# Kernel optimization log

Measured on AMD Instinct MI355X. Metric: run time of the kernel, lower is better.

The kernel has to match this reference:

```python
import jax, jax.numpy as jnp
import numpy as np

T, N, E = 4, 20000, 640000
D_IN, D_OUT = 256, 128
RRELU_SLOPE = (1.0 / 8.0 + 1.0 / 3.0) / 2.0  # RReLU eval-mode slope


def setup_inputs() -> dict:
    key = jax.random.key(0)
    ks = jax.random.split(key, 16)

    def glorot(k, shape):
        lim = np.sqrt(6.0 / (shape[0] + shape[1]))
        return jax.random.uniform(k, shape, jnp.float32, -lim, lim)

    node_embs = jax.random.normal(ks[0], (T, N, D_IN), jnp.float32)
    edge_index = jax.random.randint(ks[1], (T, 2, E), 0, N, jnp.int32)
    edge_weight = jax.random.uniform(ks[2], (T, E), jnp.float32)
    mask = jnp.zeros((T, N), jnp.float32)
    return {
        "node_embs": node_embs,
        "edge_index": edge_index,
        "edge_weight": edge_weight,
        "mask": mask,
        "p": glorot(ks[3], (D_IN, 1)),
        "Wz": glorot(ks[4], (D_IN, D_IN)),
        "Uz": glorot(ks[5], (D_IN, D_IN)),
        "bz": jnp.zeros((D_IN, D_OUT), jnp.float32),
        "Wr": glorot(ks[6], (D_IN, D_IN)),
        "Ur": glorot(ks[7], (D_IN, D_IN)),
        "br": jnp.zeros((D_IN, D_OUT), jnp.float32),
        "Wh": glorot(ks[8], (D_IN, D_IN)),
        "Uh": glorot(ks[9], (D_IN, D_IN)),
        "bh": jnp.zeros((D_IN, D_OUT), jnp.float32),
        "W0": glorot(ks[10], (D_IN, D_OUT)),
    }


def reference(node_embs, edge_index, edge_weight, mask, p, Wz, Uz, bz, Wr, Ur, br, Wh, Uh, bh, W0):
    n = node_embs.shape[1]
    k = W0.shape[1]

    def step(W, inputs):
        x, ei, w, m = inputs  # x: [N, D_IN]
        # --- TopK summary (EvolveGCN-H) ---
        scores = (x @ p)[:, 0] / jnp.linalg.norm(p) + m  # [N]
        vals, idx = jax.lax.top_k(scores, k)
        xt = (x[idx] * jnp.tanh(vals)[:, None]).T  # [D_IN, k]
        # --- matrix GRU cell: hidden state is the GCN weight W ---
        z = jax.nn.sigmoid(Wz @ xt + Uz @ W + bz)
        r = jax.nn.sigmoid(Wr @ xt + Ur @ W + br)
        h = jnp.tanh(Wh @ xt + Uh @ (r * W) + bh)
        Wn = (1.0 - z) * W + z * h  # [D_IN, D_OUT]
        # --- sparse GCN conv: adj @ (x @ Wn) ---
        y = x @ Wn  # [N, D_OUT]
        dst, src = ei[0], ei[1]
        agg = jax.ops.segment_sum(w[:, None] * y[src], dst, num_segments=n)
        out = jnp.where(agg >= 0, agg, RRELU_SLOPE * agg)
        return Wn, out

    _, out_seq = jax.lax.scan(step, W0, (node_embs, edge_index, edge_weight, mask))
    return out_seq  # [T, N, D_OUT]
```

## Files before the change

kernel.cpp:

```cpp
#include <hip/hip_runtime.h>

typedef unsigned short u16;
typedef unsigned int u32;
typedef unsigned long long u64;

#define T_ 4
#define N_ 20000
#define E_ 640000
#define DIN 256
#define DOUT 128
#define NT (T_*N_)
#define TE (T_*E_)
#define SLOPE 0.22916666666666666f

#define NB 125
#define BNODES 160
#define CAP 5632
#define NBTOT (T_*NB)

#define SGRAN 11
#define NSB 10
#define NBIN (BNODES*NSB)
#define NBIN_PAD 2048

typedef __attribute__((ext_vector_type(8))) short short8;
typedef __attribute__((ext_vector_type(4))) float f32x4;

__device__ __forceinline__ float blo(u32 u) { return __uint_as_float(u << 16); }
__device__ __forceinline__ float bhi(u32 u) { return __uint_as_float(u & 0xFFFF0000u); }
__device__ __forceinline__ u16 f2bf(float f) {
    u32 u = __float_as_uint(f);
    return (u16)((u + 0x7FFFu + ((u >> 16) & 1u)) >> 16);
}
__device__ __forceinline__ u32 fkey(float f) {
    u32 u = __float_as_uint(f);
    return (u & 0x80000000u) ? ~u : (u | 0x80000000u);
}
__device__ __forceinline__ float fkeyinv(u32 k) {
    u32 u = (k & 0x80000000u) ? (k ^ 0x80000000u) : ~k;
    return __uint_as_float(u);
}

__global__ void k_transpose(const float* Wz, const float* Uz, const float* Wr, const float* Ur,
                            const float* Wh, const float* Uh, u32* Tp) {
    int bid = blockIdx.x;
    int m = bid >> 7, b = bid & 127;
    int idx = b * 256 + threadIdx.x;
    int d2 = idx & 127, i = idx >> 7;
    const float* src;
    switch (m) {
        case 0: src = Wz; break;
        case 1: src = Uz; break;
        case 2: src = Wr; break;
        case 3: src = Ur; break;
        case 4: src = Wh; break;
        default: src = Uh; break;
    }
    float lo = src[i * 256 + 2 * d2];
    float hi = src[i * 256 + 2 * d2 + 1];
    Tp[m * 32768 + d2 * 256 + i] = (u32)f2bf(lo) | ((u32)f2bf(hi) << 16);
}

__global__ __launch_bounds__(256) void k_scores(const float* x, const float* p, const float* mask,
                                                float* scores, u16* xb16) {
    __shared__ float pl[256];
    __shared__ float s_invn;
    int tid = threadIdx.x;
    pl[tid] = p[tid];
    __syncthreads();
    if (tid < 64) {
        float v = pl[tid] * pl[tid] + pl[tid + 64] * pl[tid + 64] +
                  pl[tid + 128] * pl[tid + 128] + pl[tid + 192] * pl[tid + 192];
        for (int o = 32; o > 0; o >>= 1) v += __shfl_xor(v, o);
        if (tid == 0) s_invn = 1.0f / sqrtf(v);
    }
    __syncthreads();
    int wid = tid >> 6, lane = tid & 63;
    for (int it = 0; it < 4; ++it) {
        int node = blockIdx.x * 16 + wid * 4 + it;
        const float* row = x + (size_t)node * DIN + lane * 4;
        float4 u = *(const float4*)row;
        float d = u.x * pl[lane * 4 + 0] + u.y * pl[lane * 4 + 1] +
                  u.z * pl[lane * 4 + 2] + u.w * pl[lane * 4 + 3];
        u32 p0 = (u32)f2bf(u.x) | ((u32)f2bf(u.y) << 16);
        u32 p1 = (u32)f2bf(u.z) | ((u32)f2bf(u.w) << 16);
        *(uint2*)(xb16 + (size_t)node * DIN + lane * 4) = make_uint2(p0, p1);
        for (int o = 32; o > 0; o >>= 1) d += __shfl_xor(d, o);
        if (lane == 0) scores[node] = d * s_invn + mask[node];
    }
}

__global__ __launch_bounds__(256) void k_bin(const int* ei, const float* ew,
                                             int* gcur, uint2* binned) {
    int blk = blockIdx.x;
    int t = blk / 250, ci = blk - t * 250;
    int ebase = ci * 2560;
    int tid = threadIdx.x;
    __shared__ u32 hist[128], sc[128], gbase[128];
    __shared__ uint2 stage[2560];
    if (tid < 128) hist[tid] = 0;
    __syncthreads();
    u32 px[10]; u32 pw[10]; u16 rk[10];
#pragma unroll
    for (int k = 0; k < 10; ++k) {
        int e = ebase + tid + k * 256;
        int dst = ei[t * (2 * E_) + e];
        int src = ei[t * (2 * E_) + E_ + e];
        float w = ew[t * E_ + e];
        int b = dst / BNODES;
        int dl = dst - b * BNODES;
        px[k] = (u32)(t * N_ + src) | ((u32)dl << 17) | ((u32)b << 25);
        pw[k] = __float_as_uint(w);
        rk[k] = (u16)atomicAdd(&hist[b], 1u);
    }
    __syncthreads();
    if (tid < 128) sc[tid] = hist[tid];
    __syncthreads();
    for (int o = 1; o < 128; o <<= 1) {
        u32 v = 0;
        if (tid < 128) { v = sc[tid]; if (tid >= o) v += sc[tid - o]; }
        __syncthreads();
        if (tid < 128) sc[tid] = v;
        __syncthreads();
    }
    if (tid < NB) gbase[tid] = (u32)atomicAdd(&gcur[t * NB + tid], (int)hist[tid]);
#pragma unroll
    for (int k = 0; k < 10; ++k) {
        int b = px[k] >> 25;
        u32 slot = (sc[b] - hist[b]) + rk[k];
        stage[slot] = make_uint2(px[k], pw[k]);
    }
    __syncthreads();
    for (int s = tid; s < 2560; s += 256) {
        uint2 v = stage[s];
        int b = v.x >> 25;
        u32 local = gbase[b] + ((u32)s - (sc[b] - hist[b]));
        if (local < CAP)
            binned[(size_t)(t * NB + b) * CAP + local] = v;
    }
}

__global__ __launch_bounds__(512) void k_scatter(const int* gcur, uint2* binned, int* offsets) {
    int bg = blockIdx.x;
    int t = bg / NB, bl = bg - t * NB;
    uint2* bucket = binned + (size_t)bg * CAP;
    int cnt = gcur[bg]; if (cnt > CAP) cnt = CAP;
    int tid = threadIdx.x;
    int tbase = t * N_;
    __shared__ u32 nhist[NBIN_PAD];
    __shared__ u32 binstart[NBIN_PAD];
    __shared__ u32 wsum[8];
    for (int i = tid; i < NBIN_PAD; i += 512) nhist[i] = 0;
    __syncthreads();
    u32 vx[11]; u32 vw[11]; u16 r_[11]; u16 bn_[11];
#pragma unroll
    for (int k = 0; k < 11; ++k) {
        int e = tid + k * 512;
        r_[k] = 0xFFFFu;
        if (e < cnt) {
            uint2 v = bucket[e];
            vx[k] = v.x; vw[k] = v.y;
            int dl = (v.x >> 17) & 255;
            int s = (int)(v.x & 0x1FFFFu) - tbase;
            int bin = dl * NSB + (s >> SGRAN);
            bn_[k] = (u16)bin;
            r_[k] = (u16)atomicAdd(&nhist[bin], 1u);
        }
    }
    __syncthreads();
    u32 loc1, loc2, loc3, tsum;
    {
        int b0 = tid * 4;
        u32 a = nhist[b0], b = nhist[b0 + 1], c = nhist[b0 + 2], d = nhist[b0 + 3];
        loc1 = a; loc2 = a + b; loc3 = a + b + c; tsum = a + b + c + d;
    }
    int lane = tid & 63, wv = tid >> 6;
    u32 xsc = tsum;
    for (int o = 1; o < 64; o <<= 1) { u32 yv = __shfl_up(xsc, o); if (lane >= o) xsc += yv; }
    if (lane == 63) wsum[wv] = xsc;
    __syncthreads();
    u32 wpre = 0;
    for (int wq = 0; wq < wv; ++wq) wpre += wsum[wq];
    u32 tpre = wpre + xsc - tsum;
    {
        int b0 = tid * 4;
        binstart[b0] = tpre;
        binstart[b0 + 1] = tpre + loc1;
        binstart[b0 + 2] = tpre + loc2;
        binstart[b0 + 3] = tpre + loc3;
    }
    __syncthreads();
    if (tid < BNODES)
        offsets[t * N_ + bl * BNODES + tid] = bg * CAP + (int)binstart[tid * NSB];
    if (bg == NBTOT - 1 && tid == 0) offsets[NT] = NBTOT * CAP;
#pragma unroll
    for (int k = 0; k < 11; ++k) {
        if (r_[k] != 0xFFFFu) {
            u32 pos = binstart[bn_[k]] + r_[k];
            bucket[pos] = make_uint2(vx[k] & 0x1FFFFu, vw[k]);
        }
    }
    for (int s2 = cnt + tid; s2 < CAP; s2 += 512) bucket[s2] = make_uint2(0u, 0u);
}

__global__ __launch_bounds__(1024) void k_topk(const float* scores, const float* x, float* xtT) {
    int t = blockIdx.x;
    int tid = threadIdx.x;
    const float* sc = scores + t * N_;
    __shared__ u32 hist[256];
    __shared__ u32 sh_dig, sh_need;
    __shared__ u64 sel[256];
    __shared__ u32 selCount;
    __shared__ u32 idxl[128];
    __shared__ float tvl[128];

    u32 kreg[20];
#pragma unroll
    for (int p = 0; p < 20; ++p) {
        int i = tid + p * 1024;
        kreg[p] = (i < N_) ? fkey(sc[i]) : 0u;
    }

    u32 pref = 0;
    u32 need = 128;
    for (int pass = 0; pass < 4; ++pass) {
        int shift = 24 - 8 * pass;
        if (tid < 256) hist[tid] = 0;
        __syncthreads();
#pragma unroll
        for (int p = 0; p < 20; ++p) {
            int i = tid + p * 1024;
            u32 k = kreg[p];
            bool ok = (i < N_) && ((pass == 0) || ((k >> (shift + 8)) == pref));
            if (ok) atomicAdd(&hist[(k >> shift) & 255u], 1u);
        }
        __syncthreads();
        if (tid < 64) {
            int l = tid;
            u32 s = hist[4 * l] + hist[4 * l + 1] + hist[4 * l + 2] + hist[4 * l + 3];
            u32 S = s;
            for (int o = 1; o < 64; o <<= 1) {
                u32 y = __shfl_down(S, o);
                if (l + o < 64) S += y;
            }
            u64 m = __ballot(S >= need);
            int L = 63 - __builtin_clzll(m);
            if (l == L) {
                u32 Snext = S - s;
                u32 r = 0;
                for (int dd = 3; dd >= 0; --dd) {
                    u32 hb = hist[4 * L + dd];
                    r += hb;
                    if (Snext + r >= need) {
                        sh_dig = (u32)(4 * L + dd);
                        sh_need = need - (Snext + r - hb);
                        break;
                    }
                }
            }
        }
        __syncthreads();
        pref = (pref << 8) | sh_dig;
        need = sh_need;
        __syncthreads();
    }
    if (tid == 0) selCount = 0;
    __syncthreads();
    u32 theta = pref;
#pragma unroll
    for (int p = 0; p < 20; ++p) {
        int i = tid + p * 1024;
        u32 k = kreg[p];
        if (i < N_ && k >= theta) {
            u32 pos = atomicAdd(&selCount, 1u);
            if (pos < 256) sel[pos] = (((u64)(k ^ 0xFFFFFFFFu)) << 32) | (u32)i;
        }
    }
    __syncthreads();
    u32 c = selCount;
    if (c > 256) c = 256;
    if (tid < 256 && (u32)tid >= c) sel[tid] = 0xFFFFFFFFFFFFFFFFull;
    __syncthreads();
    for (int k2 = 2; k2 <= 256; k2 <<= 1) {
        for (int jj = k2 >> 1; jj > 0; jj >>= 1) {
            if (tid < 256) {
                int i = tid, ixj = i ^ jj;
                if (ixj > i) {
                    u64 A = sel[i], B = sel[ixj];
                    bool asc = ((i & k2) == 0);
                    bool sw = asc ? (A > B) : (A < B);
                    if (sw) { sel[i] = B; sel[ixj] = A; }
                }
            }
            __syncthreads();
        }
    }
    if (tid < 128) {
        u64 v = sel[tid];
        u32 k = ((u32)(v >> 32)) ^ 0xFFFFFFFFu;
        idxl[tid] = (u32)(v & 0xFFFFFFFFu);
        tvl[tid] = tanhf(fkeyinv(k));
    }
    __syncthreads();
    float* xt_t = xtT + t * (DIN * DOUT);
    const float* xb = x + (size_t)t * N_ * DIN;
    for (int e2 = tid; e2 < DIN * DOUT; e2 += 1024) {
        int j = e2 >> 8, d = e2 & 255;
        xt_t[e2] = xb[(size_t)idxl[j] * DIN + d] * tvl[j];
    }
}

__global__ __launch_bounds__(256) void k_gru(const float* xtT, const float* WprevT,
                                             const float* W0, int firstT, const u32* Tp,
                                             const float* bz, const float* br, const float* bh,
                                             float* WnextT, u16* WnT_t) {
    int j0 = blockIdx.x;
    int j1 = j0 + 64;
    int i = threadIdx.x;
    __shared__ float sxt[2][256], sW[2][256], srw[2][256];
    sxt[0][i] = xtT[j0 * 256 + i];
    sxt[1][i] = xtT[j1 * 256 + i];
    float wv0 = firstT ? W0[i * 128 + j0] : WprevT[j0 * 256 + i];
    float wv1 = firstT ? W0[i * 128 + j1] : WprevT[j1 * 256 + i];
    sW[0][i] = wv0;
    sW[1][i] = wv1;
    __syncthreads();
    const u32* WzT = Tp;
    const u32* UzT = Tp + 32768;
    const u32* WrT = Tp + 65536;
    const u32* UrT = Tp + 98304;
    const u32* WhT = Tp + 131072;
    const u32* UhT = Tp + 163840;
    float az0 = bz[i * 128 + j0], az1 = bz[i * 128 + j1];
    float ar0 = br[i * 128 + j0], ar1 = br[i * 128 + j1];
#pragma unroll 4
    for (int d2 = 0; d2 < 128; ++d2) {
        float x00 = sxt[0][2 * d2], x01 = sxt[0][2 * d2 + 1];
        float x10 = sxt[1][2 * d2], x11 = sxt[1][2 * d2 + 1];
        float w00 = sW[0][2 * d2], w01 = sW[0][2 * d2 + 1];
        float w10 = sW[1][2 * d2], w11 = sW[1][2 * d2 + 1];
        u32 a = WzT[d2 * 256 + i], b = UzT[d2 * 256 + i];
        u32 cc = WrT[d2 * 256 + i], dd = UrT[d2 * 256 + i];
        az0 += blo(a) * x00 + bhi(a) * x01 + blo(b) * w00 + bhi(b) * w01;
        az1 += blo(a) * x10 + bhi(a) * x11 + blo(b) * w10 + bhi(b) * w11;
        ar0 += blo(cc) * x00 + bhi(cc) * x01 + blo(dd) * w00 + bhi(dd) * w01;
        ar1 += blo(cc) * x10 + bhi(cc) * x11 + blo(dd) * w10 + bhi(dd) * w11;
    }
    float z0 = 1.0f / (1.0f + expf(-az0));
    float z1 = 1.0f / (1.0f + expf(-az1));
    float r0 = 1.0f / (1.0f + expf(-ar0));
    float r1 = 1.0f / (1.0f + expf(-ar1));
    srw[0][i] = r0 * wv0;
    srw[1][i] = r1 * wv1;
    __syncthreads();
    float ah0 = bh[i * 128 + j0], ah1 = bh[i * 128 + j1];
#pragma unroll 4
    for (int d2 = 0; d2 < 128; ++d2) {
        float x00 = sxt[0][2 * d2], x01 = sxt[0][2 * d2 + 1];
        float x10 = sxt[1][2 * d2], x11 = sxt[1][2 * d2 + 1];
        float r00 = srw[0][2 * d2], r01 = srw[0][2 * d2 + 1];
        float r10 = srw[1][2 * d2], r11 = srw[1][2 * d2 + 1];
        u32 a = WhT[d2 * 256 + i], b = UhT[d2 * 256 + i];
        ah0 += blo(a) * x00 + bhi(a) * x01 + blo(b) * r00 + bhi(b) * r01;
        ah1 += blo(a) * x10 + bhi(a) * x11 + blo(b) * r10 + bhi(b) * r11;
    }
    float h0 = tanhf(ah0), h1 = tanhf(ah1);
    float wn0 = (1.0f - z0) * wv0 + z0 * h0;
    float wn1 = (1.0f - z1) * wv1 + z1 * h1;
    WnextT[j0 * 256 + i] = wn0;
    WnextT[j1 * 256 + i] = wn1;
    WnT_t[j0 * 256 + i] = f2bf(wn0);
    WnT_t[j1 * 256 + i] = f2bf(wn1);
}

__global__ __launch_bounds__(128) void k_gemm(const u16* xb16, const u16* WnT, u16* y) {
    int t = blockIdx.y;
    const u16* xb = xb16 + (size_t)t * N_ * DIN;
    const u16* Bt = WnT + t * (DIN * DOUT);
    u16* yb = y + (size_t)t * N_ * DOUT;
    int wid = threadIdx.x >> 6, lane = threadIdx.x & 63;
    int quad = lane >> 4, lm = lane & 15;
    int rowBase = blockIdx.x * 64 + wid * 32;
    f32x4 acc[2][8];
#pragma unroll
    for (int mi = 0; mi < 2; ++mi)
#pragma unroll
        for (int ni = 0; ni < 8; ++ni) acc[mi][ni] = (f32x4){0.f, 0.f, 0.f, 0.f};
    size_t aoff[2];
#pragma unroll
    for (int mi = 0; mi < 2; ++mi) {
        int r = rowBase + mi * 16 + lm;
        if (r > N_ - 1) r = N_ - 1;
        aoff[mi] = (size_t)r * DIN + quad * 8;
    }
    const u16* bbase = Bt + lm * 256 + quad * 8;
    for (int kk = 0; kk < 256; kk += 32) {
        short8 a0 = *(const short8*)(xb + aoff[0] + kk);
        short8 a1 = *(const short8*)(xb + aoff[1] + kk);
#pragma unroll
        for (int ni = 0; ni < 8; ++ni) {
            short8 b = *(const short8*)(bbase + ni * 4096 + kk);
            acc[0][ni] = __builtin_amdgcn_mfma_f32_16x16x32_bf16(a0, b, acc[0][ni], 0, 0, 0);
            acc[1][ni] = __builtin_amdgcn_mfma_f32_16x16x32_bf16(a1, b, acc[1][ni], 0, 0, 0);
        }
    }
#pragma unroll
    for (int mi = 0; mi < 2; ++mi)
#pragma unroll
        for (int ni = 0; ni < 8; ++ni)
#pragma unroll
            for (int r = 0; r < 4; ++r) {
                int row = rowBase + mi * 16 + quad * 4 + r;
                if (row < N_) yb[(size_t)row * DOUT + ni * 16 + lm] = f2bf(acc[mi][ni][r]);
            }
}

#define ACC8(wv, v)                                             \
    acc[0] += wv * blo(v.x); acc[1] += wv * bhi(v.x);           \
    acc[2] += wv * blo(v.y); acc[3] += wv * bhi(v.y);           \
    acc[4] += wv * blo(v.z); acc[5] += wv * bhi(v.z);           \
    acc[6] += wv * blo(v.w); acc[7] += wv * bhi(v.w);

__global__ __launch_bounds__(256) void k_agg(const int* offsets, const uint2* srcw,
                                             const u16* y, float* out) {
    int nb = (blockIdx.x & 7) * 2500 + (blockIdx.x >> 3);
    int g = nb * 4 + (threadIdx.x >> 6);
    int lane = threadIdx.x & 63;
    int q = lane >> 4, lq = lane & 15;
    int o0 = offsets[g], o1 = offsets[g + 1];
    float acc[8];
#pragma unroll
    for (int i = 0; i < 8; ++i) acc[i] = 0.f;
    int e0 = o0;
    for (; e0 + 16 <= o1; e0 += 16) {
        uint2 m0 = srcw[e0 + q];
        uint2 m1 = srcw[e0 + 4 + q];
        uint2 m2 = srcw[e0 + 8 + q];
        uint2 m3 = srcw[e0 + 12 + q];
        uint4 v0 = *(const uint4*)(y + (size_t)m0.x * DOUT + lq * 8);
        uint4 v1 = *(const uint4*)(y + (size_t)m1.x * DOUT + lq * 8);
        uint4 v2 = *(const uint4*)(y + (size_t)m2.x * DOUT + lq * 8);
        uint4 v3 = *(const uint4*)(y + (size_t)m3.x * DOUT + lq * 8);
        float w0 = __uint_as_float(m0.y);
        float w1 = __uint_as_float(m1.y);
        float w2 = __uint_as_float(m2.y);
        float w3 = __uint_as_float(m3.y);
        ACC8(w0, v0)
        ACC8(w1, v1)
        ACC8(w2, v2)
        ACC8(w3, v3)
    }
    for (; e0 + 8 <= o1; e0 += 8) {
        uint2 ma = srcw[e0 + q];
        uint2 mb = srcw[e0 + 4 + q];
        uint4 va = *(const uint4*)(y + (size_t)ma.x * DOUT + lq * 8);
        uint4 vb = *(const uint4*)(y + (size_t)mb.x * DOUT + lq * 8);
        float wa = __uint_as_float(ma.y);
        float wb = __uint_as_float(mb.y);
        ACC8(wa, va)
        ACC8(wb, vb)
    }
    for (; e0 < o1; e0 += 4) {
        int e = e0 + q;
        if (e < o1) {
            uint2 m = srcw[e];
            float wv = __uint_as_float(m.y);
            uint4 v = *(const uint4*)(y + (size_t)m.x * DOUT + lq * 8);
            ACC8(wv, v)
        }
    }
#pragma unroll
    for (int i = 0; i < 8; ++i) {
        acc[i] += __shfl_xor(acc[i], 16);
        acc[i] += __shfl_xor(acc[i], 32);
        acc[i] = (acc[i] >= 0.f) ? acc[i] : SLOPE * acc[i];
    }
    if (q == 0) {
        float4 v0 = make_float4(acc[0], acc[1], acc[2], acc[3]);
        float4 v1 = make_float4(acc[4], acc[5], acc[6], acc[7]);
        float* ob = out + (size_t)g * DOUT + lq * 8;
        *(float4*)ob = v0;
        *(float4*)(ob + 4) = v1;
    }
}

extern "C" void kernel_launch(void* const* d_in, const int* in_sizes, int n_in,
                              void* d_out, int out_size, void* d_ws, size_t ws_size,
                              hipStream_t stream) {
    const float* x = (const float*)d_in[0];
    const int* ei = (const int*)d_in[1];
    const float* ew = (const float*)d_in[2];
    const float* mask = (const float*)d_in[3];
    const float* p = (const float*)d_in[4];
    const float* Wz = (const float*)d_in[5];
    const float* Uz = (const float*)d_in[6];
    const float* bz = (const float*)d_in[7];
    const float* Wr = (const float*)d_in[8];
    const float* Ur = (const float*)d_in[9];
    const float* br = (const float*)d_in[10];
    const float* Wh = (const float*)d_in[11];
    const float* Uh = (const float*)d_in[12];
    const float* bh = (const float*)d_in[13];
    const float* W0 = (const float*)d_in[14];
    float* out = (float*)d_out;

    char* w = (char*)d_ws;
    u16* xb16 = (u16*)w;        w += (size_t)NT * DIN * 2;
    float* scores = (float*)w;  w += 320256;
    float* xtT = (float*)w;     w += 4 * 32768 * 4;
    float* Wst = (float*)w;     w += 2 * 32768 * 4;
    u16* WnT = (u16*)w;         w += 4 * 32768 * 2;
    u32* Tp = (u32*)w;          w += 6 * 32768 * 4;
    u16* y = (u16*)w;           w += (size_t)NT * DOUT * 2;
    uint2* binned = (uint2*)w;  w += (size_t)NBTOT * CAP * 8;
    int* gcur = (int*)w;        w += 2048;
    int* offsets = (int*)w;     w += 320256;

    hipMemsetAsync(gcur, 0, 2048, stream);

    k_transpose<<<768, 256, 0, stream>>>(Wz, Uz, Wr, Ur, Wh, Uh, Tp);
    k_scores<<<5000, 256, 0, stream>>>(x, p, mask, scores, xb16);
    k_bin<<<1000, 256, 0, stream>>>(ei, ew, gcur, binned);
    k_scatter<<<NBTOT, 512, 0, stream>>>(gcur, binned, offsets);
    k_topk<<<4, 1024, 0, stream>>>(scores, x, xtT);

    for (int t = 0; t < 4; ++t) {
        const float* WprevT = (t == 0) ? Wst : (Wst + ((t + 1) & 1) * 32768);
        float* WnextT = Wst + (t & 1) * 32768;
        k_gru<<<64, 256, 0, stream>>>(xtT + t * 32768, WprevT, W0, (t == 0) ? 1 : 0, Tp,
                                      bz, br, bh, WnextT, WnT + t * 32768);
    }
    k_gemm<<<dim3(313, 4), 128, 0, stream>>>(xb16, WnT, y);
    k_agg<<<N_, 256, 0, stream>>>(offsets, binned, y, out);
}
```

Before: 462.1 us.

## Re-bin edges by source band and aggregate per bucket in LDS; fuse GRU steps

The scatter pass now sorts each bucket's edges by source band first and destination second, pads unused slots with dummy zero-weight edges, and records per-band, per-wave offsets. Aggregation is restructured so one block handles a whole 160-node bucket. Each wave owns 20 destination rows accumulated in shared memory and walks edges grouped by source band, which is meant to improve locality of y gathers. The four GRU launches are fused into one kernel that carries W in registers across timesteps, removing launch overhead and the global W round trip. The risks are that each wave handles one edge per iteration with 4-byte gathers per lane, and only 500 blocks of work remain for aggregation.

```diff
diff --git a/kernel.cpp b/kernel.cpp
--- a/kernel.cpp
+++ b/kernel.cpp
@@ -20,7 +20,7 @@
 
 #define SGRAN 11
 #define NSB 10
-#define NBIN (BNODES*NSB)
+#define NBIN (NSB*BNODES)
 #define NBIN_PAD 2048
 
 typedef __attribute__((ext_vector_type(8))) short short8;
@@ -140,9 +140,9 @@
     }
 }
 
-__global__ __launch_bounds__(512) void k_scatter(const int* gcur, uint2* binned, int* offsets) {
+__global__ __launch_bounds__(512) void k_scatter(const int* gcur, uint2* binned, int* bandoff) {
     int bg = blockIdx.x;
-    int t = bg / NB, bl = bg - t * NB;
+    int t = bg / NB;
     uint2* bucket = binned + (size_t)bg * CAP;
     int cnt = gcur[bg]; if (cnt > CAP) cnt = CAP;
     int tid = threadIdx.x;
@@ -156,16 +156,18 @@
 #pragma unroll
     for (int k = 0; k < 11; ++k) {
         int e = tid + k * 512;
-        r_[k] = 0xFFFFu;
+        uint2 v;
         if (e < cnt) {
-            uint2 v = bucket[e];
-            vx[k] = v.x; vw[k] = v.y;
-            int dl = (v.x >> 17) & 255;
-            int s = (int)(v.x & 0x1FFFFu) - tbase;
-            int bin = dl * NSB + (s >> SGRAN);
-            bn_[k] = (u16)bin;
-            r_[k] = (u16)atomicAdd(&nhist[bin], 1u);
-        }
+            v = bucket[e];
+        } else {
+            v = make_uint2(((u32)(e % BNODES) << 17) | (u32)(tbase + N_ - 1), 0u);
+        }
+        vx[k] = v.x; vw[k] = v.y;
+        int dl = (v.x >> 17) & 255;
+        int s = (int)(v.x & 0x1FFFFu) - tbase;
+        int bin = (s >> SGRAN) * BNODES + dl;
+        bn_[k] = (u16)bin;
+        r_[k] = (u16)atomicAdd(&nhist[bin], 1u);
     }
     __syncthreads();
     u32 loc1, loc2, loc3, tsum;
@@ -190,17 +192,13 @@
         binstart[b0 + 3] = tpre + loc3;
     }
     __syncthreads();
-    if (tid < BNODES)
-        offsets[t * N_ + bl * BNODES + tid] = bg * CAP + (int)binstart[tid * NSB];
-    if (bg == NBTOT - 1 && tid == 0) offsets[NT] = NBTOT * CAP;
+    if (tid < 80)
+        bandoff[bg * 80 + tid] = (int)binstart[(tid >> 3) * BNODES + (tid & 7) * 20];
 #pragma unroll
     for (int k = 0; k < 11; ++k) {
-        if (r_[k] != 0xFFFFu) {
-            u32 pos = binstart[bn_[k]] + r_[k];
-            bucket[pos] = make_uint2(vx[k] & 0x1FFFFu, vw[k]);
-        }
-    }
-    for (int s2 = cnt + tid; s2 < CAP; s2 += 512) bucket[s2] = make_uint2(0u, 0u);
+        u32 pos = binstart[bn_[k]] + r_[k];
+        bucket[pos] = make_uint2(vx[k] & 0x1FFFFFFu, vw[k]);
+    }
 }
 
 __global__ __launch_bounds__(1024) void k_topk(const float* scores, const float* x, float* xtT) {
@@ -310,67 +308,71 @@
     }
 }
 
-__global__ __launch_bounds__(256) void k_gru(const float* xtT, const float* WprevT,
-                                             const float* W0, int firstT, const u32* Tp,
+__global__ __launch_bounds__(256) void k_gru(const float* xtT, const float* W0, const u32* Tp,
                                              const float* bz, const float* br, const float* bh,
-                                             float* WnextT, u16* WnT_t) {
+                                             u16* WnT) {
     int j0 = blockIdx.x;
     int j1 = j0 + 64;
     int i = threadIdx.x;
     __shared__ float sxt[2][256], sW[2][256], srw[2][256];
-    sxt[0][i] = xtT[j0 * 256 + i];
-    sxt[1][i] = xtT[j1 * 256 + i];
-    float wv0 = firstT ? W0[i * 128 + j0] : WprevT[j0 * 256 + i];
-    float wv1 = firstT ? W0[i * 128 + j1] : WprevT[j1 * 256 + i];
-    sW[0][i] = wv0;
-    sW[1][i] = wv1;
-    __syncthreads();
     const u32* WzT = Tp;
     const u32* UzT = Tp + 32768;
     const u32* WrT = Tp + 65536;
     const u32* UrT = Tp + 98304;
     const u32* WhT = Tp + 131072;
     const u32* UhT = Tp + 163840;
-    float az0 = bz[i * 128 + j0], az1 = bz[i * 128 + j1];
-    float ar0 = br[i * 128 + j0], ar1 = br[i * 128 + j1];
+    float wv0 = W0[i * 128 + j0];
+    float wv1 = W0[i * 128 + j1];
+    float azb0 = bz[i * 128 + j0], azb1 = bz[i * 128 + j1];
+    float arb0 = br[i * 128 + j0], arb1 = br[i * 128 + j1];
+    float ahb0 = bh[i * 128 + j0], ahb1 = bh[i * 128 + j1];
+    for (int t = 0; t < T_; ++t) {
+        __syncthreads();
+        sxt[0][i] = xtT[t * 32768 + j0 * 256 + i];
+        sxt[1][i] = xtT[t * 32768 + j1 * 256 + i];
+        sW[0][i] = wv0;
+        sW[1][i] = wv1;
+        __syncthreads();
+        float az0 = azb0, az1 = azb1, ar0 = arb0, ar1 = arb1;
 #pragma unroll 4
-    for (int d2 = 0; d2 < 128; ++d2) {
-        float x00 = sxt[0][2 * d2], x01 = sxt[0][2 * d2 + 1];
-        float x10 = sxt[1][2 * d2], x11 = sxt[1][2 * d2 + 1];
-        float w00 = sW[0][2 * d2], w01 = sW[0][2 * d2 + 1];
-        float w10 = sW[1][2 * d2], w11 = sW[1][2 * d2 + 1];
-        u32 a = WzT[d2 * 256 + i], b = UzT[d2 * 256 + i];
-        u32 cc = WrT[d2 * 256 + i], dd = UrT[d2 * 256 + i];
-        az0 += blo(a) * x00 + bhi(a) * x01 + blo(b) * w00 + bhi(b) * w01;
-        az1 += blo(a) * x10 + bhi(a) * x11 + blo(b) * w10 + bhi(b) * w11;
-        ar0 += blo(cc) * x00 + bhi(cc) * x01 + blo(dd) * w00 + bhi(dd) * w01;
-        ar1 += blo(cc) * x10 + bhi(cc) * x11 + blo(dd) * w10 + bhi(dd) * w11;
-    }
-    float z0 = 1.0f / (1.0f + expf(-az0));
-    float z1 = 1.0f / (1.0f + expf(-az1));
-    float r0 = 1.0f / (1.0f + expf(-ar0));
-    float r1 = 1.0f / (1.0f + expf(-ar1));
-    srw[0][i] = r0 * wv0;
-    srw[1][i] = r1 * wv1;
-    __syncthreads();
-    float ah0 = bh[i * 128 + j0], ah1 = bh[i * 128 + j1];
+        for (int d2 = 0; d2 < 128; ++d2) {
+            float x00 = sxt[0][2 * d2], x01 = sxt[0][2 * d2 + 1];
+            float x10 = sxt[1][2 * d2], x11 = sxt[1][2 * d2 + 1];
+            float w00 = sW[0][2 * d2], w01 = sW[0][2 * d2 + 1];
+            float w10 = sW[1][2 * d2], w11 = sW[1][2 * d2 + 1];
+            u32 a = WzT[d2 * 256 + i], b = UzT[d2 * 256 + i];
+            u32 cc = WrT[d2 * 256 + i], dd = UrT[d2 * 256 + i];
+            az0 += blo(a) * x00 + bhi(a) * x01 + blo(b) * w00 + bhi(b) * w01;
+            az1 += blo(a) * x10 + bhi(a) * x11 + blo(b) * w10 + bhi(b) * w11;
+            ar0 += blo(cc) * x00 + bhi(cc) * x01 + blo(dd) * w00 + bhi(dd) * w01;
+            ar1 += blo(cc) * x10 + bhi(cc) * x11 + blo(dd) * w10 + bhi(dd) * w11;
+        }
+        float z0 = 1.0f / (1.0f + expf(-az0));
+        float z1 = 1.0f / (1.0f + expf(-az1));
+        float r0 = 1.0f / (1.0f + expf(-ar0));
+        float r1 = 1.0f / (1.0f + expf(-ar1));
+        srw[0][i] = r0 * wv0;
+        srw[1][i] = r1 * wv1;
+        __syncthreads();
+        float ah0 = ahb0, ah1 = ahb1;
 #pragma unroll 4
-    for (int d2 = 0; d2 < 128; ++d2) {
-        float x00 = sxt[0][2 * d2], x01 = sxt[0][2 * d2 + 1];
-        float x10 = sxt[1][2 * d2], x11 = sxt[1][2 * d2 + 1];
-        float r00 = srw[0][2 * d2], r01 = srw[0][2 * d2 + 1];
-        float r10 = srw[1][2 * d2], r11 = srw[1][2 * d2 + 1];
-        u32 a = WhT[d2 * 256 + i], b = UhT[d2 * 256 + i];
-        ah0 += blo(a) * x00 + bhi(a) * x01 + blo(b) * r00 + bhi(b) * r01;
-        ah1 += blo(a) * x10 + bhi(a) * x11 + blo(b) * r10 + bhi(b) * r11;
-    }
-    float h0 = tanhf(ah0), h1 = tanhf(ah1);
-    float wn0 = (1.0f - z0) * wv0 + z0 * h0;
-    float wn1 = (1.0f - z1) * wv1 + z1 * h1;
-    WnextT[j0 * 256 + i] = wn0;
-    WnextT[j1 * 256 + i] = wn1;
-    WnT_t[j0 * 256 + i] = f2bf(wn0);
-    WnT_t[j1 * 256 + i] = f2bf(wn1);
+        for (int d2 = 0; d2 < 128; ++d2) {
+            float x00 = sxt[0][2 * d2], x01 = sxt[0][2 * d2 + 1];
+            float x10 = sxt[1][2 * d2], x11 = sxt[1][2 * d2 + 1];
+            float r00 = srw[0][2 * d2], r01 = srw[0][2 * d2 + 1];
+            float r10 = srw[1][2 * d2], r11 = srw[1][2 * d2 + 1];
+            u32 a = WhT[d2 * 256 + i], b = UhT[d2 * 256 + i];
+            ah0 += blo(a) * x00 + bhi(a) * x01 + blo(b) * r00 + bhi(b) * r01;
+            ah1 += blo(a) * x10 + bhi(a) * x11 + blo(b) * r10 + bhi(b) * r11;
+        }
+        float h0 = tanhf(ah0), h1 = tanhf(ah1);
+        float wn0 = (1.0f - z0) * wv0 + z0 * h0;
+        float wn1 = (1.0f - z1) * wv1 + z1 * h1;
+        WnT[t * 32768 + j0 * 256 + i] = f2bf(wn0);
+        WnT[t * 32768 + j1 * 256 + i] = f2bf(wn1);
+        wv0 = wn0;
+        wv1 = wn1;
+    }
 }
 
 __global__ __launch_bounds__(128) void k_gemm(const u16* xb16, const u16* WnT, u16* y) {
@@ -415,72 +417,55 @@
             }
 }
 
-#define ACC8(wv, v)                                             \
-    acc[0] += wv * blo(v.x); acc[1] += wv * bhi(v.x);           \
-    acc[2] += wv * blo(v.y); acc[3] += wv * bhi(v.y);           \
-    acc[4] += wv * blo(v.z); acc[5] += wv * bhi(v.z);           \
-    acc[6] += wv * blo(v.w); acc[7] += wv * bhi(v.w);
-
-__global__ __launch_bounds__(256) void k_agg(const int* offsets, const uint2* srcw,
+__global__ __launch_bounds__(512) void k_agg(const uint2* binned, const int* bandoff,
                                              const u16* y, float* out) {
-    int nb = (blockIdx.x & 7) * 2500 + (blockIdx.x >> 3);
-    int g = nb * 4 + (threadIdx.x >> 6);
-    int lane = threadIdx.x & 63;
-    int q = lane >> 4, lq = lane & 15;
-    int o0 = offsets[g], o1 = offsets[g + 1];
-    float acc[8];
-#pragma unroll
-    for (int i = 0; i < 8; ++i) acc[i] = 0.f;
-    int e0 = o0;
-    for (; e0 + 16 <= o1; e0 += 16) {
-        uint2 m0 = srcw[e0 + q];
-        uint2 m1 = srcw[e0 + 4 + q];
-        uint2 m2 = srcw[e0 + 8 + q];
-        uint2 m3 = srcw[e0 + 12 + q];
-        uint4 v0 = *(const uint4*)(y + (size_t)m0.x * DOUT + lq * 8);
-        uint4 v1 = *(const uint4*)(y + (size_t)m1.x * DOUT + lq * 8);
-        uint4 v2 = *(const uint4*)(y + (size_t)m2.x * DOUT + lq * 8);
-        uint4 v3 = *(const uint4*)(y + (size_t)m3.x * DOUT + lq * 8);
-        float w0 = __uint_as_float(m0.y);
-        float w1 = __uint_as_float(m1.y);
-        float w2 = __uint_as_float(m2.y);
-        float w3 = __uint_as_float(m3.y);
-        ACC8(w0, v0)
-        ACC8(w1, v1)
-        ACC8(w2, v2)
-        ACC8(w3, v3)
-    }
-    for (; e0 + 8 <= o1; e0 += 8) {
-        uint2 ma = srcw[e0 + q];
-        uint2 mb = srcw[e0 + 4 + q];
-        uint4 va = *(const uint4*)(y + (size_t)ma.x * DOUT + lq * 8);
-        uint4 vb = *(const uint4*)(y + (size_t)mb.x * DOUT + lq * 8);
-        float wa = __uint_as_float(ma.y);
-        float wb = __uint_as_float(mb.y);
-        ACC8(wa, va)
-        ACC8(wb, vb)
-    }
-    for (; e0 < o1; e0 += 4) {
-        int e = e0 + q;
-        if (e < o1) {
-            uint2 m = srcw[e];
-            float wv = __uint_as_float(m.y);
-            uint4 v = *(const uint4*)(y + (size_t)m.x * DOUT + lq * 8);
-            ACC8(wv, v)
-        }
-    }
-#pragma unroll
-    for (int i = 0; i < 8; ++i) {
-        acc[i] += __shfl_xor(acc[i], 16);
-        acc[i] += __shfl_xor(acc[i], 32);
-        acc[i] = (acc[i] >= 0.f) ? acc[i] : SLOPE * acc[i];
-    }
-    if (q == 0) {
-        float4 v0 = make_float4(acc[0], acc[1], acc[2], acc[3]);
-        float4 v1 = make_float4(acc[4], acc[5], acc[6], acc[7]);
-        float* ob = out + (size_t)g * DOUT + lq * 8;
-        *(float4*)ob = v0;
-        *(float4*)(ob + 4) = v1;
+    int bid = blockIdx.x;
+    int xcd = bid & 7;
+    int t = xcd >> 1;
+    int bl = ((bid >> 3) << 1) + (xcd & 1);
+    if (bl >= NB) return;
+    int bg = t * NB + bl;
+    const uint2* bucket = binned + (size_t)bg * CAP;
+    const int* boff = bandoff + bg * 80;
+    int w = threadIdx.x >> 6, l = threadIdx.x & 63;
+    __shared__ float acc[8][20][128];
+#pragma unroll
+    for (int r = 0; r < 20; ++r)
+        *(float2*)&acc[w][r][2 * l] = make_float2(0.f, 0.f);
+    const u16* yl = y + 2 * l;
+    int curdl = -1;
+    float a0 = 0.f, a1 = 0.f;
+    for (int b = 0; b < NSB; ++b) {
+        int idx = b * 8 + w;
+        int e = boff[idx];
+        int eend = (idx < 79) ? boff[idx + 1] : CAP;
+        for (; e < eend; ++e) {
+            uint2 m = bucket[e];
+            int dl = (int)((m.x >> 17) & 255u);
+            if (dl != curdl) {
+                if (curdl >= 0) {
+                    float* rp = &acc[w][curdl - w * 20][2 * l];
+                    rp[0] += a0; rp[1] += a1;
+                }
+                a0 = 0.f; a1 = 0.f; curdl = dl;
+            }
+            float wt = __uint_as_float(m.y);
+            u32 yv = *(const u32*)(yl + (size_t)(m.x & 0x1FFFFu) * DOUT);
+            a0 += wt * blo(yv);
+            a1 += wt * bhi(yv);
+        }
+    }
+    if (curdl >= 0) {
+        float* rp = &acc[w][curdl - w * 20][2 * l];
+        rp[0] += a0; rp[1] += a1;
+    }
+    int gbase = t * N_ + bl * BNODES + w * 20;
+#pragma unroll
+    for (int r = 0; r < 20; ++r) {
+        float v0 = acc[w][r][2 * l], v1 = acc[w][r][2 * l + 1];
+        v0 = (v0 >= 0.f) ? v0 : SLOPE * v0;
+        v1 = (v1 >= 0.f) ? v1 : SLOPE * v1;
+        *(float2*)(out + (size_t)(gbase + r) * DOUT + 2 * l) = make_float2(v0, v1);
     }
 }
 
@@ -508,28 +493,21 @@
     u16* xb16 = (u16*)w;        w += (size_t)NT * DIN * 2;
     float* scores = (float*)w;  w += 320256;
     float* xtT = (float*)w;     w += 4 * 32768 * 4;
-    float* Wst = (float*)w;     w += 2 * 32768 * 4;
     u16* WnT = (u16*)w;         w += 4 * 32768 * 2;
     u32* Tp = (u32*)w;          w += 6 * 32768 * 4;
     u16* y = (u16*)w;           w += (size_t)NT * DOUT * 2;
     uint2* binned = (uint2*)w;  w += (size_t)NBTOT * CAP * 8;
     int* gcur = (int*)w;        w += 2048;
-    int* offsets = (int*)w;     w += 320256;
+    int* bandoff = (int*)w;     w += NBTOT * 80 * 4;
 
     hipMemsetAsync(gcur, 0, 2048, stream);
 
     k_transpose<<<768, 256, 0, stream>>>(Wz, Uz, Wr, Ur, Wh, Uh, Tp);
     k_scores<<<5000, 256, 0, stream>>>(x, p, mask, scores, xb16);
     k_bin<<<1000, 256, 0, stream>>>(ei, ew, gcur, binned);
-    k_scatter<<<NBTOT, 512, 0, stream>>>(gcur, binned, offsets);
+    k_scatter<<<NBTOT, 512, 0, stream>>>(gcur, binned, bandoff);
     k_topk<<<4, 1024, 0, stream>>>(scores, x, xtT);
-
-    for (int t = 0; t < 4; ++t) {
-        const float* WprevT = (t == 0) ? Wst : (Wst + ((t + 1) & 1) * 32768);
-        float* WnextT = Wst + (t & 1) * 32768;
-        k_gru<<<64, 256, 0, stream>>>(xtT + t * 32768, WprevT, W0, (t == 0) ? 1 : 0, Tp,
-                                      bz, br, bh, WnextT, WnT + t * 32768);
-    }
+    k_gru<<<64, 256, 0, stream>>>(xtT, W0, Tp, bz, br, bh, WnT);
     k_gemm<<<dim3(313, 4), 128, 0, stream>>>(xb16, WnT, y);
-    k_agg<<<N_, 256, 0, stream>>>(offsets, binned, y, out);
-}
+    k_agg<<<512, 512, 0, stream>>>(binned, bandoff, y, out);
+}
```

Measured after the change: 653.4 us. 41.4% more time.
